# Optimization experiments

Hardware: AMD Instinct MI355X
Metric: run time of the kernel (lower is better)

Reference implementation:

```python
import jax, jax.numpy as jnp
import numpy as np

B, N, C, H, D = 1, 256, 128, 4, 32  # batch, n_res, rep2d channels, heads, head dim


def setup_inputs() -> dict:
    key = jax.random.key(0)
    ks = jax.random.split(key, 8)
    r = lambda k, sh: jax.random.normal(k, sh, jnp.float32) * 0.02
    return {
        "x2d": jax.random.normal(ks[0], (B, N, N, C), jnp.float32),
        "norm_w": jnp.ones((C,), jnp.float32),
        "norm_b": jnp.zeros((C,), jnp.float32),
        "wq": r(ks[1], (H * D, C)),
        "wk": r(ks[2], (H * D, C)),
        "wv": r(ks[3], (H * D, C)),
        "wb": r(ks[4], (H, C)),
        "wg": r(ks[5], (H * D, C)),
        "bg": jnp.zeros((H * D,), jnp.float32),
        "wo": r(ks[6], (C, H * D)),
        "bo": jnp.zeros((C,), jnp.float32),
    }


def reference(x2d, norm_w, norm_b, wq, wk, wv, wb, wg, bg, wo, bo):
    # ending_node=False -> no transpose
    mu = jnp.mean(x2d, axis=-1, keepdims=True)
    var = jnp.var(x2d, axis=-1, keepdims=True)
    x = (x2d - mu) * jax.lax.rsqrt(var + 1e-5) * norm_w + norm_b  # LayerNorm

    q = (x @ wq.T).reshape(B, N, N, H, D)
    k = (x @ wk.T).reshape(B, N, N, H, D)
    v = (x @ wv.T).reshape(B, N, N, H, D)

    factor = 1.0 / np.sqrt(D)
    aff = jnp.einsum('bmihd,bmjhd->bmhij', q * factor, k)  # [B,M,H,I,J]

    bias = (x @ wb.T).transpose(0, 3, 1, 2)  # [B,H,I,J]
    # torch `aff + bias` broadcasts bias over the row dim m (valid since B==1)
    weights = jax.nn.softmax(aff + bias[:, None], axis=-1)

    g = jax.nn.sigmoid(x @ wg.T + bg).reshape(B, N, N, H, D)
    out = jnp.einsum('bmhqk,bmkhd->bmqhd', weights, v) * g  # gated per-head output
    out = out.reshape(B, N, N, H * D) @ wo.T + bo
    return out
```

## Files before the change

### kernel.cpp

```cpp
#include <hip/hip_runtime.h>
#include <hip/hip_bf16.h>

#define NRES 256
#define CH   128
#define NH   4
#define HD   32
#define NPX  (NRES*NRES)
#define BPX  64
#define LOG2E 1.4426950408889634f

typedef __hip_bfloat16 bf16;
typedef __attribute__((ext_vector_type(8))) short bf16x8;
typedef __attribute__((ext_vector_type(4))) float f32x4;
typedef __attribute__((ext_vector_type(16))) float f32x16;
typedef __attribute__((ext_vector_type(2))) unsigned int uint2v;

__device__ __forceinline__ float lo_f(unsigned u) { return __uint_as_float(u << 16); }
__device__ __forceinline__ float hi_f(unsigned u) { return __uint_as_float(u & 0xffff0000u); }
__device__ __forceinline__ float fexp2(float x) { return __builtin_amdgcn_exp2f(x); }
__device__ __forceinline__ unsigned pk2(float a, float b) {
    unsigned short ua = __bfloat16_as_ushort(__float2bfloat16(a));
    unsigned short ub = __bfloat16_as_ushort(__float2bfloat16(b));
    return (unsigned)ua | ((unsigned)ub << 16);
}

__global__ __launch_bounds__(256) void prep_kernel(const float* __restrict__ wq,
                                                   const float* __restrict__ wk,
                                                   const float* __restrict__ wv,
                                                   const float* __restrict__ wg,
                                                   const float* __restrict__ wo,
                                                   bf16* __restrict__ dst) {
    int mat = blockIdx.x >> 4;
    int off = ((blockIdx.x & 15) * 256 + threadIdx.x) * 4;
    const float* srcs[5] = {wq, wk, wv, wg, wo};
    float4 v4 = *reinterpret_cast<const float4*>(srcs[mat] + off);
    uint2 o;
    o.x = pk2(v4.x, v4.y);
    o.y = pk2(v4.z, v4.w);
    *reinterpret_cast<uint2*>(dst + (size_t)mat * 16384 + off) = o;
}

__global__ __launch_bounds__(256) void proj_kernel(const float* __restrict__ x2d,
                                                   const float* __restrict__ nw,
                                                   const float* __restrict__ nb,
                                                   const bf16* __restrict__ wgt,
                                                   const float* __restrict__ bg,
                                                   const float* __restrict__ wb,
                                                   bf16* __restrict__ q,
                                                   bf16* __restrict__ k,
                                                   bf16* __restrict__ v,
                                                   bf16* __restrict__ g,
                                                   float* __restrict__ bias) {
    __shared__ short xsb[BPX][128];
    int t = threadIdx.x;
    size_t pbase = (size_t)blockIdx.x * BPX;
    int px = t >> 2, lo = t & 3;

    const float* xrow = x2d + (pbase + px) * CH;
    float4 v4[8];
    #pragma unroll
    for (int cc = 0; cc < 8; ++cc)
        v4[cc] = *reinterpret_cast<const float4*>(xrow + 16 * cc + 4 * lo);

    float s = 0.f, ss = 0.f;
    #pragma unroll
    for (int cc = 0; cc < 8; ++cc) {
        s  += v4[cc].x + v4[cc].y + v4[cc].z + v4[cc].w;
        ss += v4[cc].x * v4[cc].x + v4[cc].y * v4[cc].y
            + v4[cc].z * v4[cc].z + v4[cc].w * v4[cc].w;
    }
    s += __shfl_xor(s, 1); ss += __shfl_xor(ss, 1);
    s += __shfl_xor(s, 2); ss += __shfl_xor(ss, 2);
    float mu  = s * (1.0f / CH);
    float var = ss * (1.0f / CH) - mu * mu;
    float rs  = rsqrtf(var + 1e-5f);

    #pragma unroll
    for (int cc = 0; cc < 8; ++cc) {
        int c0 = 16 * cc + 4 * lo;
        float4 wv = *reinterpret_cast<const float4*>(nw + c0);
        float4 bv = *reinterpret_cast<const float4*>(nb + c0);
        v4[cc].x = (v4[cc].x - mu) * rs * wv.x + bv.x;
        v4[cc].y = (v4[cc].y - mu) * rs * wv.y + bv.y;
        v4[cc].z = (v4[cc].z - mu) * rs * wv.z + bv.z;
        v4[cc].w = (v4[cc].w - mu) * rs * wv.w + bv.w;
        int sc = ((((c0 >> 3) ^ px) & 7) << 3) | (c0 & 7) | (c0 & 64);
        uint2 pw;
        pw.x = pk2(v4[cc].x, v4[cc].y);
        pw.y = pk2(v4[cc].z, v4[cc].w);
        *reinterpret_cast<uint2*>(&xsb[px][sc]) = pw;
    }

    float bp0 = 0.f, bp1 = 0.f, bp2 = 0.f, bp3 = 0.f;
    #pragma unroll
    for (int cc = 0; cc < 8; ++cc) {
        int c0 = 16 * cc + 4 * lo;
        float4 w0 = *reinterpret_cast<const float4*>(wb + 0 * CH + c0);
        float4 w1 = *reinterpret_cast<const float4*>(wb + 1 * CH + c0);
        float4 w2 = *reinterpret_cast<const float4*>(wb + 2 * CH + c0);
        float4 w3 = *reinterpret_cast<const float4*>(wb + 3 * CH + c0);
        bp0 += v4[cc].x * w0.x + v4[cc].y * w0.y + v4[cc].z * w0.z + v4[cc].w * w0.w;
        bp1 += v4[cc].x * w1.x + v4[cc].y * w1.y + v4[cc].z * w1.z + v4[cc].w * w1.w;
        bp2 += v4[cc].x * w2.x + v4[cc].y * w2.y + v4[cc].z * w2.z + v4[cc].w * w2.w;
        bp3 += v4[cc].x * w3.x + v4[cc].y * w3.y + v4[cc].z * w3.z + v4[cc].w * w3.w;
    }
    bp0 += __shfl_xor(bp0, 1); bp0 += __shfl_xor(bp0, 2);
    bp1 += __shfl_xor(bp1, 1); bp1 += __shfl_xor(bp1, 2);
    bp2 += __shfl_xor(bp2, 1); bp2 += __shfl_xor(bp2, 2);
    bp3 += __shfl_xor(bp3, 1); bp3 += __shfl_xor(bp3, 2);
    {
        float bv = (lo == 0) ? bp0 : (lo == 1) ? bp1 : (lo == 2) ? bp2 : bp3;
        bias[(size_t)lo * NPX + pbase + px] = bv * LOG2E;
    }
    __syncthreads();

    int w  = t >> 6, l = t & 63;
    int ll = l & 15, lg = l >> 4;
    bf16* Os[4] = {q, k, v, g};
    const float qscale = 0.17677669529663689f * LOG2E;

    #pragma unroll
    for (int mat = 0; mat < 4; ++mat) {
        const bf16* W = wgt + (size_t)mat * 16384;
        bf16x8 bfr[2][4];
        #pragma unroll
        for (int p = 0; p < 2; ++p)
            #pragma unroll
            for (int kt = 0; kt < 4; ++kt)
                bfr[p][kt] = *reinterpret_cast<const bf16x8*>(
                    W + (size_t)((2 * w + p) * 16 + ll) * CH + kt * 32 + lg * 8);

        f32x4 acc[4][2];
        #pragma unroll
        for (int mt = 0; mt < 4; ++mt)
            #pragma unroll
            for (int p = 0; p < 2; ++p) acc[mt][p] = (f32x4){0.f, 0.f, 0.f, 0.f};

        #pragma unroll
        for (int kt = 0; kt < 4; ++kt) {
            bf16x8 a[4];
            #pragma unroll
            for (int mt = 0; mt < 4; ++mt) {
                int row = 16 * mt + ll;
                int gr  = (kt * 4 + lg) ^ (row & 7);
                a[mt] = *reinterpret_cast<const bf16x8*>(&xsb[row][gr * 8]);
            }
            #pragma unroll
            for (int mt = 0; mt < 4; ++mt)
                #pragma unroll
                for (int p = 0; p < 2; ++p)
                    acc[mt][p] = __builtin_amdgcn_mfma_f32_16x16x32_bf16(a[mt], bfr[p][kt], acc[mt][p], 0, 0, 0);
        }

        #pragma unroll
        for (int p = 0; p < 2; ++p) {
            int o = (2 * w + p) * 16 + ll;
            float bgv = (mat == 3) ? bg[o] : 0.f;
            #pragma unroll
            for (int mt = 0; mt < 4; ++mt) {
                #pragma unroll
                for (int r = 0; r < 4; ++r) {
                    int prow = 16 * mt + lg * 4 + r;
                    float valf = acc[mt][p][r];
                    if (mat == 0) valf *= qscale;
                    if (mat == 3) valf = 1.f / (1.f + __expf(-(valf + bgv)));
                    Os[mat][(pbase + prow) * CH + o] = __float2bfloat16(valf);
                }
            }
        }
    }
}

__global__ __launch_bounds__(256, 4) void attn_kernel(const bf16* q,
                                                      const bf16* __restrict__ kk,
                                                      const bf16* __restrict__ vv,
                                                      const float* __restrict__ bias,
                                                      const bf16* __restrict__ gg,
                                                      bf16* attn) {
    __shared__ short vt[HD][NRES];

    int t   = threadIdx.x;
    int w   = t >> 6;
    int l   = t & 63;
    int l31 = l & 31;
    int hi5 = l >> 5;
    int m = blockIdx.x, h = blockIdx.y;
    size_t base = ((size_t)m * NRES) * CH + (size_t)h * HD;

    for (int it = 0; it < 4; ++it) {
        int e8 = t + 256 * it;
        int j  = e8 >> 2;
        int d0 = (e8 & 3) * 8;
        uint4 vu = *reinterpret_cast<const uint4*>(vv + base + (size_t)j * CH + d0);
        union { uint4 u; short s[8]; } vc; vc.u = vu;
        #pragma unroll
        for (int s = 0; s < 8; ++s)
            vt[d0 + s][j ^ (8 * s)] = vc.s[s];
    }

    bf16x8 qf[2][2];
    #pragma unroll
    for (int ig = 0; ig < 2; ++ig)
        #pragma unroll
        for (int tt = 0; tt < 2; ++tt)
            qf[ig][tt] = *reinterpret_cast<const bf16x8*>(
                q + base + (size_t)(w * 64 + ig * 32 + l31) * CH + tt * 16 + hi5 * 8);

    __syncthreads();

    float m_run[2] = {-1e30f, -1e30f};
    float l_run[2] = {0.f, 0.f};
    f32x16 oacc[2];
    #pragma unroll
    for (int ig = 0; ig < 2; ++ig)
        #pragma unroll
        for (int r = 0; r < 16; ++r) oacc[ig][r] = 0.f;

    const float* bh = bias + (size_t)h * NPX;

    for (int jt = 0; jt < 8; ++jt) {
        int j0 = jt * 32;

        bf16x8 kf0 = *reinterpret_cast<const bf16x8*>(kk + base + (size_t)(j0 + l31) * CH + hi5 * 8);
        bf16x8 kf1 = *reinterpret_cast<const bf16x8*>(kk + base + (size_t)(j0 + l31) * CH + 16 + hi5 * 8);

        f32x16 sac[2];
        #pragma unroll
        for (int ig = 0; ig < 2; ++ig) {
            f32x16 zz;
            #pragma unroll
            for (int r = 0; r < 16; ++r) zz[r] = 0.f;
            zz = __builtin_amdgcn_mfma_f32_32x32x16_bf16(kf0, qf[ig][0], zz, 0, 0, 0);
            sac[ig] = __builtin_amdgcn_mfma_f32_32x32x16_bf16(kf1, qf[ig][1], zz, 0, 0, 0);
        }

        __builtin_amdgcn_s_setprio(1);
        #pragma unroll
        for (int ig = 0; ig < 2; ++ig) {
            int i = w * 64 + ig * 32 + l31;
            #pragma unroll
            for (int rq = 0; rq < 4; ++rq) {
                float4 b4 = *reinterpret_cast<const float4*>(bh + (size_t)i * NRES + j0 + 8 * rq + 4 * hi5);
                sac[ig][4 * rq + 0] += b4.x; sac[ig][4 * rq + 1] += b4.y;
                sac[ig][4 * rq + 2] += b4.z; sac[ig][4 * rq + 3] += b4.w;
            }
        }
        __builtin_amdgcn_s_setprio(0);

        #pragma unroll
        for (int ig = 0; ig < 2; ++ig) {
            float a0 = fmaxf(sac[ig][0], sac[ig][1]),  a1 = fmaxf(sac[ig][2], sac[ig][3]);
            float a2 = fmaxf(sac[ig][4], sac[ig][5]),  a3 = fmaxf(sac[ig][6], sac[ig][7]);
            float a4 = fmaxf(sac[ig][8], sac[ig][9]),  a5 = fmaxf(sac[ig][10], sac[ig][11]);
            float a6 = fmaxf(sac[ig][12], sac[ig][13]), a7 = fmaxf(sac[ig][14], sac[ig][15]);
            float mx = fmaxf(fmaxf(fmaxf(a0, a1), fmaxf(a2, a3)), fmaxf(fmaxf(a4, a5), fmaxf(a6, a7)));
            mx = fmaxf(mx, __shfl_xor(mx, 32));

            if (!__all(mx <= m_run[ig] + 8.f)) {
                float mnew = fmaxf(m_run[ig], mx);
                float sc = fexp2(m_run[ig] - mnew);
                l_run[ig] *= sc;
                #pragma unroll
                for (int r = 0; r < 16; ++r) oacc[ig][r] *= sc;
                m_run[ig] = mnew;
            }
            float mm = m_run[ig];
            #pragma unroll
            for (int r = 0; r < 16; ++r) sac[ig][r] = fexp2(sac[ig][r] - mm);
            float s0 = sac[ig][0] + sac[ig][1],  s1 = sac[ig][2] + sac[ig][3];
            float s2 = sac[ig][4] + sac[ig][5],  s3 = sac[ig][6] + sac[ig][7];
            float s4 = sac[ig][8] + sac[ig][9],  s5 = sac[ig][10] + sac[ig][11];
            float s6 = sac[ig][12] + sac[ig][13], s7 = sac[ig][14] + sac[ig][15];
            float psum = ((s0 + s1) + (s2 + s3)) + ((s4 + s5) + (s6 + s7));
            psum += __shfl_xor(psum, 32);
            l_run[ig] += psum;
        }

        #pragma unroll
        for (int tt = 0; tt < 2; ++tt) {
            bf16x8 vf = *reinterpret_cast<const bf16x8*>(
                &vt[l31][(j0 + 16 * tt + 8 * hi5) ^ (8 * (l31 & 7))]);
            #pragma unroll
            for (int ig = 0; ig < 2; ++ig) {
                unsigned x0 = pk2(sac[ig][8 * tt + 0], sac[ig][8 * tt + 1]);
                unsigned x1 = pk2(sac[ig][8 * tt + 2], sac[ig][8 * tt + 3]);
                unsigned y0 = pk2(sac[ig][8 * tt + 4], sac[ig][8 * tt + 5]);
                unsigned y1 = pk2(sac[ig][8 * tt + 6], sac[ig][8 * tt + 7]);
                uint2v r0 = __builtin_amdgcn_permlane32_swap(x0, y0, false, false);
                uint2v r1 = __builtin_amdgcn_permlane32_swap(x1, y1, false, false);
                union { unsigned u[4]; bf16x8 v; } pf;
                pf.u[0] = r0[0];
                pf.u[1] = r1[0];
                pf.u[2] = r0[1];
                pf.u[3] = r1[1];
                oacc[ig] = __builtin_amdgcn_mfma_f32_32x32x16_bf16(vf, pf.v, oacc[ig], 0, 0, 0);
            }
        }
    }

    #pragma unroll
    for (int ig = 0; ig < 2; ++ig) {
        float inv = 1.f / l_run[ig];
        size_t prow = base + (size_t)(w * 64 + ig * 32 + l31) * CH;
        #pragma unroll
        for (int rq = 0; rq < 4; ++rq) {
            int d0 = 8 * rq + 4 * hi5;
            uint2 gu = *reinterpret_cast<const uint2*>(gg + prow + d0);
            float g0 = lo_f(gu.x), g1 = hi_f(gu.x), g2 = lo_f(gu.y), g3 = hi_f(gu.y);
            uint2 ow;
            ow.x = pk2(oacc[ig][4 * rq + 0] * inv * g0, oacc[ig][4 * rq + 1] * inv * g1);
            ow.y = pk2(oacc[ig][4 * rq + 2] * inv * g2, oacc[ig][4 * rq + 3] * inv * g3);
            *reinterpret_cast<uint2*>(attn + prow + d0) = ow;
        }
    }
}

__global__ __launch_bounds__(256) void out_kernel(const bf16* __restrict__ ga,
                                                  const bf16* __restrict__ wob,
                                                  const float* __restrict__ bo,
                                                  float* __restrict__ out) {
    __shared__ short xsb[BPX][128];
    int t = threadIdx.x;
    size_t pbase = (size_t)blockIdx.x * BPX;

    for (int it = 0; it < 4; ++it) {
        int idx = (it * 256 + t) * 8;
        int px = idx >> 7, c = idx & 127;
        int gr = c >> 3;
        uint4 u = *reinterpret_cast<const uint4*>(ga + pbase * CH + idx);
        *reinterpret_cast<uint4*>(&xsb[px][(gr ^ (px & 7)) * 8]) = u;
    }
    __syncthreads();

    int w  = t >> 6, l = t & 63;
    int ll = l & 15, lg = l >> 4;

    bf16x8 bfr[2][4];
    #pragma unroll
    for (int p = 0; p < 2; ++p)
        #pragma unroll
        for (int kt = 0; kt < 4; ++kt)
            bfr[p][kt] = *reinterpret_cast<const bf16x8*>(
                wob + (size_t)((2 * w + p) * 16 + ll) * CH + kt * 32 + lg * 8);

    f32x4 acc[4][2];
    #pragma unroll
    for (int mt = 0; mt < 4; ++mt)
        #pragma unroll
        for (int p = 0; p < 2; ++p) acc[mt][p] = (f32x4){0.f, 0.f, 0.f, 0.f};

    #pragma unroll
    for (int kt = 0; kt < 4; ++kt) {
        bf16x8 a[4];
        #pragma unroll
        for (int mt = 0; mt < 4; ++mt) {
            int row = 16 * mt + ll;
            int gr  = (kt * 4 + lg) ^ (row & 7);
            a[mt] = *reinterpret_cast<const bf16x8*>(&xsb[row][gr * 8]);
        }
        #pragma unroll
        for (int mt = 0; mt < 4; ++mt)
            #pragma unroll
            for (int p = 0; p < 2; ++p)
                acc[mt][p] = __builtin_amdgcn_mfma_f32_16x16x32_bf16(a[mt], bfr[p][kt], acc[mt][p], 0, 0, 0);
    }

    #pragma unroll
    for (int p = 0; p < 2; ++p) {
        int o = (2 * w + p) * 16 + ll;
        float bov = bo[o];
        #pragma unroll
        for (int mt = 0; mt < 4; ++mt)
            #pragma unroll
            for (int r = 0; r < 4; ++r) {
                int prow = 16 * mt + lg * 4 + r;
                out[(pbase + prow) * CH + o] = acc[mt][p][r] + bov;
            }
    }
}

extern "C" void kernel_launch(void* const* d_in, const int* in_sizes, int n_in,
                              void* d_out, int out_size, void* d_ws, size_t ws_size,
                              hipStream_t stream) {
    const float* x2d = (const float*)d_in[0];
    const float* nw  = (const float*)d_in[1];
    const float* nb  = (const float*)d_in[2];
    const float* wq  = (const float*)d_in[3];
    const float* wk  = (const float*)d_in[4];
    const float* wv  = (const float*)d_in[5];
    const float* wb  = (const float*)d_in[6];
    const float* wg  = (const float*)d_in[7];
    const float* bg  = (const float*)d_in[8];
    const float* wo  = (const float*)d_in[9];
    const float* bo  = (const float*)d_in[10];
    float* out = (float*)d_out;

    float* bias = (float*)d_ws;
    bf16*  q    = (bf16*)((float*)d_ws + (size_t)NH * NPX);
    bf16*  k    = q + (size_t)NPX * CH;
    bf16*  v    = k + (size_t)NPX * CH;
    bf16*  g    = v + (size_t)NPX * CH;
    bf16*  wgt  = g + (size_t)NPX * CH;
    bf16*  wob  = wgt + 4 * 16384;

    prep_kernel<<<80, 256, 0, stream>>>(wq, wk, wv, wg, wo, wgt);
    proj_kernel<<<NPX / BPX, 256, 0, stream>>>(x2d, nw, nb, wgt, bg, wb, q, k, v, g, bias);
    attn_kernel<<<dim3(NRES, NH), 256, 0, stream>>>(q, k, v, bias, g, q);
    out_kernel<<<NPX / BPX, 256, 0, stream>>>(q, wob, bo, out);
}
```

Baseline: 107.3 us.

## Split attention query rows across grid z and pre-transpose bias for coalesced reads

Adds a kernel that transposes the per-head pair bias so the attention kernel can read it with lanes walking along the query index. Each attention block now handles 128 query rows, with one 32-row group per wave, and the grid gains a z dimension of 2. This doubles the number of blocks, and the launch bound is raised to 8 blocks per CU so occupancy can rise with fewer live registers per thread. The cost is that each block stages V into shared memory twice as often, the extra transpose launch adds traffic, and the bias loads become 16 scalar loads per tile instead of float4 loads.

```diff
diff --git a/kernel.cpp b/kernel.cpp
--- a/kernel.cpp
+++ b/kernel.cpp
@@ -171,10 +171,45 @@
     }
 }
 
-__global__ __launch_bounds__(256, 4) void attn_kernel(const bf16* q,
+__global__ __launch_bounds__(256) void tbias_kernel(const float* __restrict__ bias,
+                                                    float* __restrict__ biasT) {
+    __shared__ float tileT[64][65];
+    int h  = blockIdx.x >> 4;
+    int it = (blockIdx.x >> 2) & 3;
+    int jt = blockIdx.x & 3;
+    int t  = threadIdx.x;
+    int r  = t >> 4;
+    int c0 = (t & 15) * 4;
+
+    const float* src = bias + (size_t)h * NPX + (size_t)(it * 64) * NRES + jt * 64;
+    #pragma unroll
+    for (int rr = 0; rr < 4; ++rr) {
+        int row = r + 16 * rr;
+        float4 f4 = *reinterpret_cast<const float4*>(src + (size_t)row * NRES + c0);
+        tileT[c0 + 0][row] = f4.x;
+        tileT[c0 + 1][row] = f4.y;
+        tileT[c0 + 2][row] = f4.z;
+        tileT[c0 + 3][row] = f4.w;
+    }
+    __syncthreads();
+
+    float* dst = biasT + (size_t)h * NPX + (size_t)(jt * 64) * NRES + it * 64;
+    #pragma unroll
+    for (int rr = 0; rr < 4; ++rr) {
+        int row = r + 16 * rr;
+        float4 o4;
+        o4.x = tileT[row][c0 + 0];
+        o4.y = tileT[row][c0 + 1];
+        o4.z = tileT[row][c0 + 2];
+        o4.w = tileT[row][c0 + 3];
+        *reinterpret_cast<float4*>(dst + (size_t)row * NRES + c0) = o4;
+    }
+}
+
+__global__ __launch_bounds__(256, 8) void attn_kernel(const bf16* q,
                                                       const bf16* __restrict__ kk,
                                                       const bf16* __restrict__ vv,
-                                                      const float* __restrict__ bias,
+                                                      const float* __restrict__ biasT,
                                                       const bf16* __restrict__ gg,
                                                       bf16* attn) {
     __shared__ short vt[HD][NRES];
@@ -184,8 +219,9 @@
     int l   = t & 63;
     int l31 = l & 31;
     int hi5 = l >> 5;
-    int m = blockIdx.x, h = blockIdx.y;
+    int m = blockIdx.x, h = blockIdx.y, z = blockIdx.z;
     size_t base = ((size_t)m * NRES) * CH + (size_t)h * HD;
+    int ibase = z * 128 + w * 32;
 
     for (int it = 0; it < 4; ++it) {
         int e8 = t + 256 * it;
@@ -198,25 +234,17 @@
             vt[d0 + s][j ^ (8 * s)] = vc.s[s];
     }
 
-    bf16x8 qf[2][2];
-    #pragma unroll
-    for (int ig = 0; ig < 2; ++ig)
-        #pragma unroll
-        for (int tt = 0; tt < 2; ++tt)
-            qf[ig][tt] = *reinterpret_cast<const bf16x8*>(
-                q + base + (size_t)(w * 64 + ig * 32 + l31) * CH + tt * 16 + hi5 * 8);
+    bf16x8 qf0 = *reinterpret_cast<const bf16x8*>(q + base + (size_t)(ibase + l31) * CH + hi5 * 8);
+    bf16x8 qf1 = *reinterpret_cast<const bf16x8*>(q + base + (size_t)(ibase + l31) * CH + 16 + hi5 * 8);
 
     __syncthreads();
 
-    float m_run[2] = {-1e30f, -1e30f};
-    float l_run[2] = {0.f, 0.f};
-    f32x16 oacc[2];
-    #pragma unroll
-    for (int ig = 0; ig < 2; ++ig)
-        #pragma unroll
-        for (int r = 0; r < 16; ++r) oacc[ig][r] = 0.f;
-
-    const float* bh = bias + (size_t)h * NPX;
+    float m_run = -1e30f, l_run = 0.f;
+    f32x16 oacc;
+    #pragma unroll
+    for (int r = 0; r < 16; ++r) oacc[r] = 0.f;
+
+    const float* bT = biasT + (size_t)h * NPX;
 
     for (int jt = 0; jt < 8; ++jt) {
         int j0 = jt * 32;
@@ -224,92 +252,77 @@
         bf16x8 kf0 = *reinterpret_cast<const bf16x8*>(kk + base + (size_t)(j0 + l31) * CH + hi5 * 8);
         bf16x8 kf1 = *reinterpret_cast<const bf16x8*>(kk + base + (size_t)(j0 + l31) * CH + 16 + hi5 * 8);
 
-        f32x16 sac[2];
-        #pragma unroll
-        for (int ig = 0; ig < 2; ++ig) {
-            f32x16 zz;
-            #pragma unroll
-            for (int r = 0; r < 16; ++r) zz[r] = 0.f;
-            zz = __builtin_amdgcn_mfma_f32_32x32x16_bf16(kf0, qf[ig][0], zz, 0, 0, 0);
-            sac[ig] = __builtin_amdgcn_mfma_f32_32x32x16_bf16(kf1, qf[ig][1], zz, 0, 0, 0);
-        }
-
-        __builtin_amdgcn_s_setprio(1);
-        #pragma unroll
-        for (int ig = 0; ig < 2; ++ig) {
-            int i = w * 64 + ig * 32 + l31;
-            #pragma unroll
-            for (int rq = 0; rq < 4; ++rq) {
-                float4 b4 = *reinterpret_cast<const float4*>(bh + (size_t)i * NRES + j0 + 8 * rq + 4 * hi5);
-                sac[ig][4 * rq + 0] += b4.x; sac[ig][4 * rq + 1] += b4.y;
-                sac[ig][4 * rq + 2] += b4.z; sac[ig][4 * rq + 3] += b4.w;
-            }
-        }
-        __builtin_amdgcn_s_setprio(0);
-
-        #pragma unroll
-        for (int ig = 0; ig < 2; ++ig) {
-            float a0 = fmaxf(sac[ig][0], sac[ig][1]),  a1 = fmaxf(sac[ig][2], sac[ig][3]);
-            float a2 = fmaxf(sac[ig][4], sac[ig][5]),  a3 = fmaxf(sac[ig][6], sac[ig][7]);
-            float a4 = fmaxf(sac[ig][8], sac[ig][9]),  a5 = fmaxf(sac[ig][10], sac[ig][11]);
-            float a6 = fmaxf(sac[ig][12], sac[ig][13]), a7 = fmaxf(sac[ig][14], sac[ig][15]);
+        f32x16 sac;
+        #pragma unroll
+        for (int r = 0; r < 16; ++r) sac[r] = 0.f;
+        sac = __builtin_amdgcn_mfma_f32_32x32x16_bf16(kf0, qf0, sac, 0, 0, 0);
+        sac = __builtin_amdgcn_mfma_f32_32x32x16_bf16(kf1, qf1, sac, 0, 0, 0);
+
+        #pragma unroll
+        for (int r = 0; r < 16; ++r) {
+            int jl = (r & 3) + 8 * (r >> 2) + 4 * hi5;
+            sac[r] += bT[(size_t)(j0 + jl) * NRES + ibase + l31];
+        }
+
+        {
+            float a0 = fmaxf(sac[0], sac[1]),  a1 = fmaxf(sac[2], sac[3]);
+            float a2 = fmaxf(sac[4], sac[5]),  a3 = fmaxf(sac[6], sac[7]);
+            float a4 = fmaxf(sac[8], sac[9]),  a5 = fmaxf(sac[10], sac[11]);
+            float a6 = fmaxf(sac[12], sac[13]), a7 = fmaxf(sac[14], sac[15]);
             float mx = fmaxf(fmaxf(fmaxf(a0, a1), fmaxf(a2, a3)), fmaxf(fmaxf(a4, a5), fmaxf(a6, a7)));
             mx = fmaxf(mx, __shfl_xor(mx, 32));
 
-            if (!__all(mx <= m_run[ig] + 8.f)) {
-                float mnew = fmaxf(m_run[ig], mx);
-                float sc = fexp2(m_run[ig] - mnew);
-                l_run[ig] *= sc;
+            if (!__all(mx <= m_run + 8.f)) {
+                float mnew = fmaxf(m_run, mx);
+                float sc = fexp2(m_run - mnew);
+                l_run *= sc;
                 #pragma unroll
-                for (int r = 0; r < 16; ++r) oacc[ig][r] *= sc;
-                m_run[ig] = mnew;
+                for (int r = 0; r < 16; ++r) oacc[r] *= sc;
+                m_run = mnew;
             }
-            float mm = m_run[ig];
-            #pragma unroll
-            for (int r = 0; r < 16; ++r) sac[ig][r] = fexp2(sac[ig][r] - mm);
-            float s0 = sac[ig][0] + sac[ig][1],  s1 = sac[ig][2] + sac[ig][3];
-            float s2 = sac[ig][4] + sac[ig][5],  s3 = sac[ig][6] + sac[ig][7];
-            float s4 = sac[ig][8] + sac[ig][9],  s5 = sac[ig][10] + sac[ig][11];
-            float s6 = sac[ig][12] + sac[ig][13], s7 = sac[ig][14] + sac[ig][15];
+            #pragma unroll
+            for (int r = 0; r < 16; ++r) sac[r] = fexp2(sac[r] - m_run);
+            float s0 = sac[0] + sac[1],  s1 = sac[2] + sac[3];
+            float s2 = sac[4] + sac[5],  s3 = sac[6] + sac[7];
+            float s4 = sac[8] + sac[9],  s5 = sac[10] + sac[11];
+            float s6 = sac[12] + sac[13], s7 = sac[14] + sac[15];
             float psum = ((s0 + s1) + (s2 + s3)) + ((s4 + s5) + (s6 + s7));
             psum += __shfl_xor(psum, 32);
-            l_run[ig] += psum;
-        }
-
+            l_run += psum;
+        }
+
+        __builtin_amdgcn_s_setprio(1);
         #pragma unroll
         for (int tt = 0; tt < 2; ++tt) {
             bf16x8 vf = *reinterpret_cast<const bf16x8*>(
                 &vt[l31][(j0 + 16 * tt + 8 * hi5) ^ (8 * (l31 & 7))]);
-            #pragma unroll
-            for (int ig = 0; ig < 2; ++ig) {
-                unsigned x0 = pk2(sac[ig][8 * tt + 0], sac[ig][8 * tt + 1]);
-                unsigned x1 = pk2(sac[ig][8 * tt + 2], sac[ig][8 * tt + 3]);
-                unsigned y0 = pk2(sac[ig][8 * tt + 4], sac[ig][8 * tt + 5]);
-                unsigned y1 = pk2(sac[ig][8 * tt + 6], sac[ig][8 * tt + 7]);
-                uint2v r0 = __builtin_amdgcn_permlane32_swap(x0, y0, false, false);
-                uint2v r1 = __builtin_amdgcn_permlane32_swap(x1, y1, false, false);
-                union { unsigned u[4]; bf16x8 v; } pf;
-                pf.u[0] = r0[0];
-                pf.u[1] = r1[0];
-                pf.u[2] = r0[1];
-                pf.u[3] = r1[1];
-                oacc[ig] = __builtin_amdgcn_mfma_f32_32x32x16_bf16(vf, pf.v, oacc[ig], 0, 0, 0);
-            }
-        }
-    }
-
-    #pragma unroll
-    for (int ig = 0; ig < 2; ++ig) {
-        float inv = 1.f / l_run[ig];
-        size_t prow = base + (size_t)(w * 64 + ig * 32 + l31) * CH;
+            unsigned x0 = pk2(sac[8 * tt + 0], sac[8 * tt + 1]);
+            unsigned x1 = pk2(sac[8 * tt + 2], sac[8 * tt + 3]);
+            unsigned y0 = pk2(sac[8 * tt + 4], sac[8 * tt + 5]);
+            unsigned y1 = pk2(sac[8 * tt + 6], sac[8 * tt + 7]);
+            uint2v r0 = __builtin_amdgcn_permlane32_swap(x0, y0, false, false);
+            uint2v r1 = __builtin_amdgcn_permlane32_swap(x1, y1, false, false);
+            union { unsigned u[4]; bf16x8 v; } pf;
+            pf.u[0] = r0[0];
+            pf.u[1] = r1[0];
+            pf.u[2] = r0[1];
+            pf.u[3] = r1[1];
+            oacc = __builtin_amdgcn_mfma_f32_32x32x16_bf16(vf, pf.v, oacc, 0, 0, 0);
+        }
+        __builtin_amdgcn_s_setprio(0);
+    }
+
+    {
+        float inv = 1.f / l_run;
+        size_t prow = base + (size_t)(ibase + l31) * CH;
         #pragma unroll
         for (int rq = 0; rq < 4; ++rq) {
             int d0 = 8 * rq + 4 * hi5;
             uint2 gu = *reinterpret_cast<const uint2*>(gg + prow + d0);
             float g0 = lo_f(gu.x), g1 = hi_f(gu.x), g2 = lo_f(gu.y), g3 = hi_f(gu.y);
             uint2 ow;
-            ow.x = pk2(oacc[ig][4 * rq + 0] * inv * g0, oacc[ig][4 * rq + 1] * inv * g1);
-            ow.y = pk2(oacc[ig][4 * rq + 2] * inv * g2, oacc[ig][4 * rq + 3] * inv * g3);
+            ow.x = pk2(oacc[4 * rq + 0] * inv * g0, oacc[4 * rq + 1] * inv * g1);
+            ow.y = pk2(oacc[4 * rq + 2] * inv * g2, oacc[4 * rq + 3] * inv * g3);
             *reinterpret_cast<uint2*>(attn + prow + d0) = ow;
         }
     }
@@ -402,9 +415,11 @@
     bf16*  g    = v + (size_t)NPX * CH;
     bf16*  wgt  = g + (size_t)NPX * CH;
     bf16*  wob  = wgt + 4 * 16384;
+    float* biasT = (float*)(wob + 16384);
 
     prep_kernel<<<80, 256, 0, stream>>>(wq, wk, wv, wg, wo, wgt);
     proj_kernel<<<NPX / BPX, 256, 0, stream>>>(x2d, nw, nb, wgt, bg, wb, q, k, v, g, bias);
-    attn_kernel<<<dim3(NRES, NH), 256, 0, stream>>>(q, k, v, bias, g, q);
+    tbias_kernel<<<64, 256, 0, stream>>>(bias, biasT);
+    attn_kernel<<<dim3(NRES, NH, 2), 256, 0, stream>>>(q, k, v, biasT, g, q);
     out_kernel<<<NPX / BPX, 256, 0, stream>>>(q, wob, bo, out);
 }
```

After: 119.0 us. 10.9% more time.

## Swap projection GEMM operands to 32x32 MFMA for vectorized row stores

Applied to the files above, without the earlier changes.

The projection and output GEMMs now use 32x32x16 MFMA with the weight as the A operand and the pixels as B. Each lane then holds contiguous output channels for one pixel, so results go out as packed 8-byte bf16 or 16-byte float4 stores instead of scattered scalar stores. Weight fragments are loaded per k-step rather than preloaded, and bias vectors are read with float4 loads. The attention kernel also raises wave priority around the PV MFMA block with s_setprio, which is meant to improve interleaving between waves.

```diff
diff --git a/kernel.cpp b/kernel.cpp
--- a/kernel.cpp
+++ b/kernel.cpp
@@ -114,59 +114,57 @@
     }
     __syncthreads();
 
-    int w  = t >> 6, l = t & 63;
-    int ll = l & 15, lg = l >> 4;
+    int w   = t >> 6, l = t & 63;
+    int l31 = l & 31, hi5 = l >> 5;
     bf16* Os[4] = {q, k, v, g};
     const float qscale = 0.17677669529663689f * LOG2E;
+    int swz = l31 & 7;
 
     #pragma unroll
     for (int mat = 0; mat < 4; ++mat) {
-        const bf16* W = wgt + (size_t)mat * 16384;
-        bf16x8 bfr[2][4];
-        #pragma unroll
-        for (int p = 0; p < 2; ++p)
-            #pragma unroll
-            for (int kt = 0; kt < 4; ++kt)
-                bfr[p][kt] = *reinterpret_cast<const bf16x8*>(
-                    W + (size_t)((2 * w + p) * 16 + ll) * CH + kt * 32 + lg * 8);
-
-        f32x4 acc[4][2];
-        #pragma unroll
-        for (int mt = 0; mt < 4; ++mt)
-            #pragma unroll
-            for (int p = 0; p < 2; ++p) acc[mt][p] = (f32x4){0.f, 0.f, 0.f, 0.f};
-
-        #pragma unroll
-        for (int kt = 0; kt < 4; ++kt) {
-            bf16x8 a[4];
-            #pragma unroll
-            for (int mt = 0; mt < 4; ++mt) {
-                int row = 16 * mt + ll;
-                int gr  = (kt * 4 + lg) ^ (row & 7);
-                a[mt] = *reinterpret_cast<const bf16x8*>(&xsb[row][gr * 8]);
-            }
-            #pragma unroll
-            for (int mt = 0; mt < 4; ++mt)
-                #pragma unroll
-                for (int p = 0; p < 2; ++p)
-                    acc[mt][p] = __builtin_amdgcn_mfma_f32_16x16x32_bf16(a[mt], bfr[p][kt], acc[mt][p], 0, 0, 0);
-        }
-
-        #pragma unroll
-        for (int p = 0; p < 2; ++p) {
-            int o = (2 * w + p) * 16 + ll;
-            float bgv = (mat == 3) ? bg[o] : 0.f;
-            #pragma unroll
-            for (int mt = 0; mt < 4; ++mt) {
-                #pragma unroll
-                for (int r = 0; r < 4; ++r) {
-                    int prow = 16 * mt + lg * 4 + r;
-                    float valf = acc[mt][p][r];
-                    if (mat == 0) valf *= qscale;
-                    if (mat == 3) valf = 1.f / (1.f + __expf(-(valf + bgv)));
-                    Os[mat][(pbase + prow) * CH + o] = __float2bfloat16(valf);
-                }
-            }
+        const bf16* W = wgt + (size_t)mat * 16384 + (size_t)(w * 32 + l31) * CH;
+
+        f32x16 acc0, acc1;
+        #pragma unroll
+        for (int r = 0; r < 16; ++r) { acc0[r] = 0.f; acc1[r] = 0.f; }
+
+        #pragma unroll
+        for (int kt = 0; kt < 8; ++kt) {
+            bf16x8 af = *reinterpret_cast<const bf16x8*>(W + kt * 16 + hi5 * 8);
+            int g4 = kt * 2 + hi5;
+            bf16x8 b0 = *reinterpret_cast<const bf16x8*>(&xsb[l31][(g4 ^ swz) * 8]);
+            bf16x8 b1 = *reinterpret_cast<const bf16x8*>(&xsb[32 + l31][(g4 ^ swz) * 8]);
+            acc0 = __builtin_amdgcn_mfma_f32_32x32x16_bf16(af, b0, acc0, 0, 0, 0);
+            acc1 = __builtin_amdgcn_mfma_f32_32x32x16_bf16(af, b1, acc1, 0, 0, 0);
+        }
+
+        bf16* dst = Os[mat];
+        #pragma unroll
+        for (int rq = 0; rq < 4; ++rq) {
+            int o = w * 32 + 8 * rq + 4 * hi5;
+            float e0 = acc0[4 * rq + 0], e1 = acc0[4 * rq + 1];
+            float e2 = acc0[4 * rq + 2], e3 = acc0[4 * rq + 3];
+            float f0 = acc1[4 * rq + 0], f1 = acc1[4 * rq + 1];
+            float f2 = acc1[4 * rq + 2], f3 = acc1[4 * rq + 3];
+            if (mat == 0) {
+                e0 *= qscale; e1 *= qscale; e2 *= qscale; e3 *= qscale;
+                f0 *= qscale; f1 *= qscale; f2 *= qscale; f3 *= qscale;
+            }
+            if (mat == 3) {
+                float4 b4 = *reinterpret_cast<const float4*>(bg + o);
+                e0 = 1.f / (1.f + __expf(-(e0 + b4.x)));
+                e1 = 1.f / (1.f + __expf(-(e1 + b4.y)));
+                e2 = 1.f / (1.f + __expf(-(e2 + b4.z)));
+                e3 = 1.f / (1.f + __expf(-(e3 + b4.w)));
+                f0 = 1.f / (1.f + __expf(-(f0 + b4.x)));
+                f1 = 1.f / (1.f + __expf(-(f1 + b4.y)));
+                f2 = 1.f / (1.f + __expf(-(f2 + b4.z)));
+                f3 = 1.f / (1.f + __expf(-(f3 + b4.w)));
+            }
+            uint2 p0; p0.x = pk2(e0, e1); p0.y = pk2(e2, e3);
+            uint2 p1; p1.x = pk2(f0, f1); p1.y = pk2(f2, f3);
+            *reinterpret_cast<uint2*>(dst + (pbase + l31) * CH + o)      = p0;
+            *reinterpret_cast<uint2*>(dst + (pbase + 32 + l31) * CH + o) = p1;
         }
     }
 }
@@ -276,6 +274,7 @@
             l_run[ig] += psum;
         }
 
+        __builtin_amdgcn_s_setprio(1);
         #pragma unroll
         for (int tt = 0; tt < 2; ++tt) {
             bf16x8 vf = *reinterpret_cast<const bf16x8*>(
@@ -296,6 +295,7 @@
                 oacc[ig] = __builtin_amdgcn_mfma_f32_32x32x16_bf16(vf, pf.v, oacc[ig], 0, 0, 0);
             }
         }
+        __builtin_amdgcn_s_setprio(0);
     }
 
     #pragma unroll
@@ -332,50 +332,36 @@
     }
     __syncthreads();
 
-    int w  = t >> 6, l = t & 63;
-    int ll = l & 15, lg = l >> 4;
-
-    bf16x8 bfr[2][4];
-    #pragma unroll
-    for (int p = 0; p < 2; ++p)
-        #pragma unroll
-        for (int kt = 0; kt < 4; ++kt)
-            bfr[p][kt] = *reinterpret_cast<const bf16x8*>(
-                wob + (size_t)((2 * w + p) * 16 + ll) * CH + kt * 32 + lg * 8);
-
-    f32x4 acc[4][2];
-    #pragma unroll
-    for (int mt = 0; mt < 4; ++mt)
-        #pragma unroll
-        for (int p = 0; p < 2; ++p) acc[mt][p] = (f32x4){0.f, 0.f, 0.f, 0.f};
-
-    #pragma unroll
-    for (int kt = 0; kt < 4; ++kt) {
-        bf16x8 a[4];
-        #pragma unroll
-        for (int mt = 0; mt < 4; ++mt) {
-            int row = 16 * mt + ll;
-            int gr  = (kt * 4 + lg) ^ (row & 7);
-            a[mt] = *reinterpret_cast<const bf16x8*>(&xsb[row][gr * 8]);
-        }
-        #pragma unroll
-        for (int mt = 0; mt < 4; ++mt)
-            #pragma unroll
-            for (int p = 0; p < 2; ++p)
-                acc[mt][p] = __builtin_amdgcn_mfma_f32_16x16x32_bf16(a[mt], bfr[p][kt], acc[mt][p], 0, 0, 0);
-    }
-
-    #pragma unroll
-    for (int p = 0; p < 2; ++p) {
-        int o = (2 * w + p) * 16 + ll;
-        float bov = bo[o];
-        #pragma unroll
-        for (int mt = 0; mt < 4; ++mt)
-            #pragma unroll
-            for (int r = 0; r < 4; ++r) {
-                int prow = 16 * mt + lg * 4 + r;
-                out[(pbase + prow) * CH + o] = acc[mt][p][r] + bov;
-            }
+    int w   = t >> 6, l = t & 63;
+    int l31 = l & 31, hi5 = l >> 5;
+    int swz = l31 & 7;
+    const bf16* W = wob + (size_t)(w * 32 + l31) * CH;
+
+    f32x16 acc0, acc1;
+    #pragma unroll
+    for (int r = 0; r < 16; ++r) { acc0[r] = 0.f; acc1[r] = 0.f; }
+
+    #pragma unroll
+    for (int kt = 0; kt < 8; ++kt) {
+        bf16x8 af = *reinterpret_cast<const bf16x8*>(W + kt * 16 + hi5 * 8);
+        int g4 = kt * 2 + hi5;
+        bf16x8 b0 = *reinterpret_cast<const bf16x8*>(&xsb[l31][(g4 ^ swz) * 8]);
+        bf16x8 b1 = *reinterpret_cast<const bf16x8*>(&xsb[32 + l31][(g4 ^ swz) * 8]);
+        acc0 = __builtin_amdgcn_mfma_f32_32x32x16_bf16(af, b0, acc0, 0, 0, 0);
+        acc1 = __builtin_amdgcn_mfma_f32_32x32x16_bf16(af, b1, acc1, 0, 0, 0);
+    }
+
+    #pragma unroll
+    for (int rq = 0; rq < 4; ++rq) {
+        int o = w * 32 + 8 * rq + 4 * hi5;
+        float4 bo4 = *reinterpret_cast<const float4*>(bo + o);
+        float4 s0, s1;
+        s0.x = acc0[4 * rq + 0] + bo4.x; s0.y = acc0[4 * rq + 1] + bo4.y;
+        s0.z = acc0[4 * rq + 2] + bo4.z; s0.w = acc0[4 * rq + 3] + bo4.w;
+        s1.x = acc1[4 * rq + 0] + bo4.x; s1.y = acc1[4 * rq + 1] + bo4.y;
+        s1.z = acc1[4 * rq + 2] + bo4.z; s1.w = acc1[4 * rq + 3] + bo4.w;
+        *reinterpret_cast<float4*>(out + (pbase + l31) * CH + o)      = s0;
+        *reinterpret_cast<float4*>(out + (pbase + 32 + l31) * CH + o) = s1;
     }
 }
 
```

Measured after the change: 116.6 us. +8.7%, slower.
